# Optimization experiments

Hardware: AMD Instinct MI355X
Metric: run time of the kernel (lower is better)

## Reference

```python
import jax, jax.numpy as jnp
import numpy as np

N = 50000   # nodes
E = 800000  # edges (avg degree 16)
D = 96      # in = hid = out
BN_EPS = 1e-5


def setup_inputs() -> dict:
    key = jax.random.key(0)
    ks = jax.random.split(key, 16)
    features = jax.random.normal(ks[0], (N, D), jnp.float32)
    src = jax.random.randint(ks[1], (E,), 0, N)
    dst = jax.random.randint(ks[2], (E,), 0, N)
    bound = 1.0 / np.sqrt(D)
    def lin(kw, kb):
        W = jax.random.uniform(kw, (D, D), jnp.float32, -bound, bound)
        b = jax.random.uniform(kb, (D,), jnp.float32, -bound, bound)
        return W, b
    W1, b1 = lin(ks[3], ks[4])
    W2, b2 = lin(ks[5], ks[6])
    W3, b3 = lin(ks[7], ks[8])
    gamma1 = jnp.ones((D,), jnp.float32)
    beta1 = jnp.zeros((D,), jnp.float32)
    gamma2 = jnp.ones((D,), jnp.float32)
    beta2 = jnp.zeros((D,), jnp.float32)
    return dict(features=features, W1=W1, b1=b1, gamma1=gamma1, beta1=beta1,
                W2=W2, b2=b2, gamma2=gamma2, beta2=beta2, W3=W3, b3=b3,
                src=src, dst=dst)


def _gin_conv(h, W, b, src, dst, inv_deg):
    # mean-aggregate incoming neighbor features, eps = 0: (h + mean_nb) @ W + b
    agg = jax.ops.segment_sum(h[src], dst, num_segments=N) * inv_deg[:, None]
    return (h + agg) @ W + b


def _batchnorm(x, gamma, beta):
    mu = jnp.mean(x, axis=0)
    var = jnp.mean((x - mu) ** 2, axis=0)  # biased, as torch BN training
    return (x - mu) * jax.lax.rsqrt(var + BN_EPS) * gamma + beta


def reference(features, W1, b1, gamma1, beta1, W2, b2, gamma2, beta2, W3, b3, src, dst):
    deg = jax.ops.segment_sum(jnp.ones((E,), jnp.float32), dst, num_segments=N)
    inv_deg = jnp.where(deg > 0, 1.0 / jnp.maximum(deg, 1.0), 0.0)
    h = _gin_conv(features, W1, b1, src, dst, inv_deg)
    h = jax.nn.relu(_batchnorm(h, gamma1, beta1))  # dropout p=0 -> identity
    h = _gin_conv(h, W2, b2, src, dst, inv_deg)
    h = jax.nn.relu(_batchnorm(h, gamma2, beta2))
    h = _gin_conv(h, W3, b3, src, dst, inv_deg)
    return h
```

## Files before the change

### kernel.cpp

```cpp
#include <hip/hip_runtime.h>

#define FD 96
#define BSH 7
#define BNODES 128
#define NBLK 256

typedef float  f32x4 __attribute__((ext_vector_type(4)));
typedef short  s16x8 __attribute__((ext_vector_type(8)));

__device__ __forceinline__ unsigned short f2bf(float x) {
    unsigned u = __float_as_uint(x);
    u = (u + 0x7fffu + ((u >> 16) & 1u)) >> 16;
    return (unsigned short)u;
}
__device__ __forceinline__ float bflo(unsigned u) { return __uint_as_float(u << 16); }
__device__ __forceinline__ float bfhi(unsigned u) { return __uint_as_float(u & 0xffff0000u); }


__global__ void k_h2d(const int* __restrict__ dst, int* __restrict__ hist2d,
                      int E, int nbkt, int chunk) {
    __shared__ int hist[512];
    int tid = threadIdx.x, b = blockIdx.x;
    for (int i = tid; i < 512; i += 256) hist[i] = 0;
    __syncthreads();
    int lo = b * chunk, hi = min(lo + chunk, E);
    for (int i = lo + tid; i < hi; i += 256)
        atomicAdd(&hist[dst[i] >> BSH], 1);
    __syncthreads();
    for (int q = tid; q < nbkt; q += 256)
        hist2d[(size_t)q * NBLK + b] = hist[q];
}

__global__ void k_cscan(const int* __restrict__ hist2d, int* __restrict__ cursor2d,
                        int* __restrict__ bcnt, float* __restrict__ accz) {
    __shared__ int sh[NBLK];
    int q = blockIdx.x, tid = threadIdx.x;
    if (q == 0) for (int i = tid; i < 4 * FD; i += 256) accz[i] = 0.f;
    int v = hist2d[(size_t)q * NBLK + tid];
    sh[tid] = v;
    __syncthreads();
    for (int off = 1; off < NBLK; off <<= 1) {
        int t = (tid >= off) ? sh[tid - off] : 0;
        __syncthreads();
        sh[tid] += t;
        __syncthreads();
    }
    cursor2d[(size_t)q * NBLK + tid] = sh[tid] - v;
    if (tid == NBLK - 1) bcnt[q] = sh[tid];
}

__global__ void k_bscan(const int* __restrict__ bcnt, int* __restrict__ bbase, int nbkt) {
    __shared__ int sh[512];
    int tid = threadIdx.x;
    int v = (tid < nbkt) ? bcnt[tid] : 0;
    sh[tid] = v;
    __syncthreads();
    for (int off = 1; off < 512; off <<= 1) {
        int t = (tid >= off) ? sh[tid - off] : 0;
        __syncthreads();
        sh[tid] += t;
        __syncthreads();
    }
    int incl = sh[tid];
    if (tid < nbkt) bbase[tid] = incl - v;
    if (tid == nbkt - 1) bbase[nbkt] = incl;
}

__global__ void k_scat(const int* __restrict__ src, const int* __restrict__ dst,
                       const int* __restrict__ cursor2d, const int* __restrict__ bbase,
                       uint2* __restrict__ ebuf, int E, int nbkt, int chunk) {
    __shared__ int cur[512];
    int tid = threadIdx.x, b = blockIdx.x;
    for (int q = tid; q < nbkt; q += 256)
        cur[q] = bbase[q] + cursor2d[(size_t)q * NBLK + b];
    __syncthreads();
    int lo = b * chunk, hi = min(lo + chunk, E);
    for (int i = lo + tid; i < hi; i += 256) {
        int d = dst[i];
        int p = atomicAdd(&cur[d >> BSH], 1);
        ebuf[p] = make_uint2((unsigned)d, (unsigned)src[i]);
    }
}

__global__ void k_bsort(const uint2* __restrict__ ebuf, const int* __restrict__ bbase,
                        int* __restrict__ csr, int* __restrict__ rp2, int* __restrict__ re2,
                        float* __restrict__ invd2, int* __restrict__ perm,
                        int* __restrict__ inv_perm, int n) {
    __shared__ int cnt[BNODES];
    __shared__ int cur[BNODES];
    __shared__ int dh[64];
    const int b = blockIdx.x;
    const int tid = threadIdx.x;
    const int lo = bbase[b], hi = bbase[b + 1];
    if (tid < BNODES) cnt[tid] = 0;
    if (tid < 64) dh[tid] = 0;
    __syncthreads();
    for (int i = lo + tid; i < hi; i += blockDim.x)
        atomicAdd(&cnt[(int)ebuf[i].x - (b << BSH)], 1);
    __syncthreads();
    const int node = (b << BSH) + tid;
    const int v = (tid < BNODES) ? cnt[tid] : 0;
    const int dcl = min(v, 63);
    if (tid < BNODES && node < n) atomicAdd(&dh[dcl], 1);
    for (int off = 1; off < BNODES; off <<= 1) {
        int t = (tid < BNODES && tid >= off) ? cnt[tid - off] : 0;
        __syncthreads();
        if (tid < BNODES) cnt[tid] += t;
        __syncthreads();
    }
    int dv = (tid < 64) ? dh[tid] : 0;
    for (int off = 1; off < 64; off <<= 1) {
        int t = (tid < 64 && tid >= off) ? dh[tid - off] : 0;
        __syncthreads();
        if (tid < 64) dh[tid] += t;
        __syncthreads();
    }
    if (tid < 64) dh[tid] -= dv;
    __syncthreads();
    if (tid < BNODES) {
        int excl = cnt[tid] - v;
        if (node < n) {
            int rk = atomicAdd(&dh[dcl], 1);
            int slot = (b << BSH) + rk;
            perm[slot] = node;
            inv_perm[node] = slot;
            rp2[slot] = lo + excl;
            re2[slot] = lo + excl + v;
            invd2[slot] = (v > 0) ? (1.0f / (float)v) : 0.f;
        }
        cur[tid] = excl;
    }
    __syncthreads();
    for (int i = lo + tid; i < hi; i += blockDim.x) {
        uint2 e2 = ebuf[i];
        int local = (int)e2.x - (b << BSH);
        int p = lo + atomicAdd(&cur[local], 1);
        csr[p] = (int)e2.y;
    }
}

__global__ void k_prep(int* __restrict__ csr, const int* __restrict__ inv_perm, int E,
                       const float* __restrict__ feat, const int* __restrict__ perm,
                       uint4* __restrict__ hA, int n,
                       const float* __restrict__ W1, const float* __restrict__ W2,
                       const float* __restrict__ W3, unsigned short* __restrict__ Wt) {
    int i = blockIdx.x * blockDim.x + threadIdx.x;
    if (i < E) {
        csr[i] = inv_perm[csr[i]];
        return;
    }
    i -= E;
    const int n12 = n * 12;
    if (i < n12) {
        int row = i / 12, q = i - row * 12;
        int node = perm[row];
        const float4* rp = (const float4*)(feat + (size_t)node * FD);
        float4 x = rp[2 * q], y = rp[2 * q + 1];
        uint4 r;
        r.x = (unsigned)f2bf(x.x) | ((unsigned)f2bf(x.y) << 16);
        r.y = (unsigned)f2bf(x.z) | ((unsigned)f2bf(x.w) << 16);
        r.z = (unsigned)f2bf(y.x) | ((unsigned)f2bf(y.y) << 16);
        r.w = (unsigned)f2bf(y.z) | ((unsigned)f2bf(y.w) << 16);
        hA[i] = r;
        return;
    }
    i -= n12;
    if (i < 3 * FD * FD) {
        int m = i / (FD * FD), r = i - m * FD * FD;
        const float* W = (m == 0) ? W1 : ((m == 1) ? W2 : W3);
        int col = r % FD, k = r / FD;
        Wt[m * FD * FD + col * FD + k] = f2bf(W[r]);
    }
}


template<int NORM, int STATS, int OBF>
__global__ __launch_bounds__(256) void k_aggmm(
    const uint4* __restrict__ h,
    const int* __restrict__ rp2, const int* __restrict__ re2,
    const float* __restrict__ invd2, const int* __restrict__ csr,
    const float* __restrict__ accPrev, const float* __restrict__ gamma,
    const float* __restrict__ beta,
    const unsigned short* __restrict__ Wt, const float* __restrict__ bias,
    const int* __restrict__ perm,
    unsigned short* __restrict__ yb, float* __restrict__ yf,
    float* __restrict__ accg, int n, float invN)
{
    __shared__ uint4 t_lds[64][13];
    __shared__ float sred[2 * FD];
    const int tid = threadIdx.x;
    const int rl = tid >> 2;
    const int qq = tid & 3;
    const int idx = blockIdx.x * 64 + rl;
    const bool valid = (idx < n);
    int beg = 0, end = 0;
    float id = 0.f;
    if (valid) { beg = rp2[idx]; end = re2[idx]; id = invd2[idx]; }

    #pragma unroll 1
    for (int p = 0; p < 3; p++) {
        const int q = p * 4 + qq;
        float a[8], c[8];
        if (NORM) {
            #pragma unroll
            for (int z = 0; z < 8; z++) {
                int f = q * 8 + z;
                float mu  = accPrev[f] * invN;
                float var = accPrev[FD + f] * invN - mu * mu;
                float aa  = gamma[f] * rsqrtf(var + 1e-5f);
                a[z] = aa;
                c[z] = beta[f] - mu * aa;
            }
        }
        float o[8];
        #pragma unroll
        for (int z = 0; z < 8; z++) o[z] = 0.f;

        if (valid) {
            float acc8[8];
            #pragma unroll
            for (int z = 0; z < 8; z++) acc8[z] = 0.f;
            int e = beg;
            for (; e + 8 <= end; e += 8) {
                uint4 raw[8];
                #pragma unroll
                for (int u = 0; u < 8; u++) raw[u] = h[(size_t)csr[e + u] * 12 + q];
                #pragma unroll
                for (int u = 0; u < 8; u++) {
                    float v[8];
                    v[0] = bflo(raw[u].x); v[1] = bfhi(raw[u].x);
                    v[2] = bflo(raw[u].y); v[3] = bfhi(raw[u].y);
                    v[4] = bflo(raw[u].z); v[5] = bfhi(raw[u].z);
                    v[6] = bflo(raw[u].w); v[7] = bfhi(raw[u].w);
                    #pragma unroll
                    for (int z = 0; z < 8; z++) {
                        float x = v[z];
                        if (NORM) x = fmaxf(fmaf(a[z], x, c[z]), 0.f);
                        acc8[z] += x;
                    }
                }
            }
            for (; e < end; e++) {
                uint4 raw = h[(size_t)csr[e] * 12 + q];
                float v[8];
                v[0] = bflo(raw.x); v[1] = bfhi(raw.x);
                v[2] = bflo(raw.y); v[3] = bfhi(raw.y);
                v[4] = bflo(raw.z); v[5] = bfhi(raw.z);
                v[6] = bflo(raw.w); v[7] = bfhi(raw.w);
                #pragma unroll
                for (int z = 0; z < 8; z++) {
                    float x = v[z];
                    if (NORM) x = fmaxf(fmaf(a[z], x, c[z]), 0.f);
                    acc8[z] += x;
                }
            }
            uint4 rs = h[(size_t)idx * 12 + q];
            float xs[8];
            xs[0] = bflo(rs.x); xs[1] = bfhi(rs.x);
            xs[2] = bflo(rs.y); xs[3] = bfhi(rs.y);
            xs[4] = bflo(rs.z); xs[5] = bfhi(rs.z);
            xs[6] = bflo(rs.w); xs[7] = bfhi(rs.w);
            #pragma unroll
            for (int z = 0; z < 8; z++) {
                float x = xs[z];
                if (NORM) x = fmaxf(fmaf(a[z], x, c[z]), 0.f);
                o[z] = fmaf(id, acc8[z], x);
            }
        }
        uint4 pk;
        pk.x = (unsigned)f2bf(o[0]) | ((unsigned)f2bf(o[1]) << 16);
        pk.y = (unsigned)f2bf(o[2]) | ((unsigned)f2bf(o[3]) << 16);
        pk.z = (unsigned)f2bf(o[4]) | ((unsigned)f2bf(o[5]) << 16);
        pk.w = (unsigned)f2bf(o[6]) | ((unsigned)f2bf(o[7]) << 16);
        t_lds[rl][q] = pk;
    }
    __syncthreads();

    const int lane = tid & 63;
    const int wv   = tid >> 6;
    const int colb = lane & 15;
    const int hg   = lane >> 4;
    const int rbase = blockIdx.x * 64 + wv * 16;

    s16x8 a[3];
    #pragma unroll
    for (int s = 0; s < 3; s++)
        a[s] = *reinterpret_cast<const s16x8*>(&t_lds[wv * 16 + colb][s * 4 + hg]);

    s16x8 b[6][3];
    #pragma unroll
    for (int c2 = 0; c2 < 6; c2++)
        #pragma unroll
        for (int s = 0; s < 3; s++)
            b[c2][s] = *reinterpret_cast<const s16x8*>(Wt + (size_t)(c2 * 16 + colb) * FD + s * 32 + hg * 8);

    f32x4 acc[6];
    #pragma unroll
    for (int c2 = 0; c2 < 6; c2++) acc[c2] = (f32x4){0.f, 0.f, 0.f, 0.f};
    #pragma unroll
    for (int s = 0; s < 3; s++)
        #pragma unroll
        for (int c2 = 0; c2 < 6; c2++)
            acc[c2] = __builtin_amdgcn_mfma_f32_16x16x32_bf16(a[s], b[c2][s], acc[c2], 0, 0, 0);

    int orow[4];
    #pragma unroll
    for (int j = 0; j < 4; j++) {
        int rr = rbase + hg * 4 + j;
        orow[j] = (!OBF && rr < n) ? perm[rr] : rr;
    }
    float s1[6], s2[6];
    #pragma unroll
    for (int c2 = 0; c2 < 6; c2++) { s1[c2] = 0.f; s2[c2] = 0.f; }
    #pragma unroll
    for (int c2 = 0; c2 < 6; c2++) {
        float bc = bias[c2 * 16 + colb];
        #pragma unroll
        for (int j = 0; j < 4; j++) {
            int rr = rbase + hg * 4 + j;
            if (rr < n) {
                float y = acc[c2][j] + bc;
                if (OBF) yb[(size_t)rr * FD + c2 * 16 + colb] = f2bf(y);
                else     yf[(size_t)orow[j] * FD + c2 * 16 + colb] = y;
                if (STATS) { s1[c2] += y; s2[c2] = fmaf(y, y, s2[c2]); }
            }
        }
    }
    if (STATS) {
        if (tid < 2 * FD) sred[tid] = 0.f;
        __syncthreads();
        #pragma unroll
        for (int c2 = 0; c2 < 6; c2++) {
            float v1 = s1[c2], v2 = s2[c2];
            v1 += __shfl_xor(v1, 16, 64); v1 += __shfl_xor(v1, 32, 64);
            v2 += __shfl_xor(v2, 16, 64); v2 += __shfl_xor(v2, 32, 64);
            if (lane < 16) {
                atomicAdd(&sred[c2 * 16 + colb], v1);
                atomicAdd(&sred[FD + c2 * 16 + colb], v2);
            }
        }
        __syncthreads();
        if (tid < 2 * FD) atomicAdd(&accg[tid], sred[tid]);
    }
}

extern "C" void kernel_launch(void* const* d_in, const int* in_sizes, int n_in,
                              void* d_out, int out_size, void* d_ws, size_t ws_size,
                              hipStream_t stream) {
    const float* feat = (const float*)d_in[0];
    const float* W1   = (const float*)d_in[1];
    const float* b1   = (const float*)d_in[2];
    const float* g1   = (const float*)d_in[3];
    const float* be1  = (const float*)d_in[4];
    const float* W2   = (const float*)d_in[5];
    const float* b2   = (const float*)d_in[6];
    const float* g2   = (const float*)d_in[7];
    const float* be2  = (const float*)d_in[8];
    const float* W3   = (const float*)d_in[9];
    const float* b3   = (const float*)d_in[10];
    const int*   src  = (const int*)d_in[11];
    const int*   dst  = (const int*)d_in[12];

    const int n = in_sizes[0] / FD;
    const int e = in_sizes[11];
    const int nbkt = (n + BNODES - 1) >> BSH;
    const int chunk = (e + NBLK - 1) / NBLK;

    char* w = (char*)d_ws;
    unsigned short* hA  = (unsigned short*)w; w += (size_t)n * FD * 2;
    unsigned short* hB  = (unsigned short*)w; w += (size_t)n * FD * 2;
    unsigned short* Wt  = (unsigned short*)w; w += (size_t)3 * FD * FD * 2;
    int*   csr     = (int*)w;   w += (size_t)e * 4;
    int*   bcnt    = (int*)w;   w += 512 * 4;
    float* acc1    = (float*)w; w += 2 * FD * 4;
    float* acc2    = (float*)w; w += 2 * FD * 4;
    int*   bbase   = (int*)w;   w += 513 * 4;
    int*   hist2d  = (int*)w;   w += (size_t)512 * NBLK * 4;
    int*   cursor2d= (int*)w;   w += (size_t)512 * NBLK * 4;
    int*   rp2     = (int*)w;   w += (size_t)n * 4;
    int*   re2     = (int*)w;   w += (size_t)n * 4;
    float* invd2   = (float*)w; w += (size_t)n * 4;
    int*   perm    = (int*)w;   w += (size_t)n * 4;
    int*   invp    = (int*)w;   w += (size_t)n * 4;

    uint2* ebuf = (uint2*)hB;

    float* O = (float*)d_out;
    const float invN = 1.0f / (float)n;
    const int FUSE_GRID = (n + 63) / 64;
    const int n12 = n * 12;
    const int prep_items = e + n12 + 3 * FD * FD;

    k_h2d<<<NBLK, 256, 0, stream>>>(dst, hist2d, e, nbkt, chunk);
    k_cscan<<<nbkt, NBLK, 0, stream>>>(hist2d, cursor2d, bcnt, acc1);
    k_bscan<<<1, 512, 0, stream>>>(bcnt, bbase, nbkt);
    k_scat<<<NBLK, 256, 0, stream>>>(src, dst, cursor2d, bbase, ebuf, e, nbkt, chunk);
    k_bsort<<<nbkt, 256, 0, stream>>>(ebuf, bbase, csr, rp2, re2, invd2, perm, invp, n);
    k_prep<<<(prep_items + 255) / 256, 256, 0, stream>>>(csr, invp, e, feat, perm,
                                                         (uint4*)hA, n, W1, W2, W3, Wt);

    k_aggmm<0, 1, 1><<<FUSE_GRID, 256, 0, stream>>>(
        (const uint4*)hA, rp2, re2, invd2, csr, nullptr, nullptr, nullptr,
        Wt, b1, perm, hB, nullptr, acc1, n, invN);

    k_aggmm<1, 1, 1><<<FUSE_GRID, 256, 0, stream>>>(
        (const uint4*)hB, rp2, re2, invd2, csr, acc1, g1, be1,
        Wt + FD * FD, b2, perm, hA, nullptr, acc2, n, invN);

    k_aggmm<1, 0, 0><<<FUSE_GRID, 256, 0, stream>>>(
        (const uint4*)hA, rp2, re2, invd2, csr, acc2, g2, be2,
        Wt + 2 * FD * FD, b3, perm, nullptr, O, nullptr, n, invN);
}
```

Before: 262.7 us.

## Split fused aggregate+matmul into separate gather and MFMA kernels

Splits each fused aggregation-plus-GEMM layer into a gather kernel that uses one thread per (row, 16-byte chunk) and a separate MFMA matmul kernel. The split intermediate goes to global memory, and one of the bf16 activation buffers now lives in the output buffer. This is meant to give the latency-bound gather full parallelism (12 lanes per row, no 3-pass loop, occupancy hint of 4 blocks) instead of serialising per block before the LDS handoff. The cost is three extra kernel launches plus a global round-trip of the aggregated tensor per layer.

```diff
diff --git a/kernel.cpp b/kernel.cpp
--- a/kernel.cpp
+++ b/kernel.cpp
@@ -174,119 +174,118 @@
 }
 
 
-template<int NORM, int STATS, int OBF>
-__global__ __launch_bounds__(256) void k_aggmm(
+template<int NORM>
+__global__ __launch_bounds__(256, 4) void k_agg(
     const uint4* __restrict__ h,
     const int* __restrict__ rp2, const int* __restrict__ re2,
     const float* __restrict__ invd2, const int* __restrict__ csr,
     const float* __restrict__ accPrev, const float* __restrict__ gamma,
-    const float* __restrict__ beta,
-    const unsigned short* __restrict__ Wt, const float* __restrict__ bias,
-    const int* __restrict__ perm,
-    unsigned short* __restrict__ yb, float* __restrict__ yf,
-    float* __restrict__ accg, int n, float invN)
+    const float* __restrict__ beta, float invN,
+    uint4* __restrict__ t, int n)
 {
-    __shared__ uint4 t_lds[64][13];
-    __shared__ float sred[2 * FD];
-    const int tid = threadIdx.x;
-    const int rl = tid >> 2;
-    const int qq = tid & 3;
-    const int idx = blockIdx.x * 64 + rl;
-    const bool valid = (idx < n);
-    int beg = 0, end = 0;
-    float id = 0.f;
-    if (valid) { beg = rp2[idx]; end = re2[idx]; id = invd2[idx]; }
-
-    #pragma unroll 1
-    for (int p = 0; p < 3; p++) {
-        const int q = p * 4 + qq;
-        float a[8], c[8];
-        if (NORM) {
+    int g = blockIdx.x * blockDim.x + threadIdx.x;
+    int row = g / 12;
+    if (row >= n) return;
+    int q = g - row * 12;
+    float a[8], c[8];
+    if (NORM) {
+        #pragma unroll
+        for (int z = 0; z < 8; z++) {
+            int f = q * 8 + z;
+            float mu  = accPrev[f] * invN;
+            float var = accPrev[FD + f] * invN - mu * mu;
+            float aa  = gamma[f] * rsqrtf(var + 1e-5f);
+            a[z] = aa;
+            c[z] = beta[f] - mu * aa;
+        }
+    }
+    float acc8[8];
+    #pragma unroll
+    for (int z = 0; z < 8; z++) acc8[z] = 0.f;
+
+    int e = rp2[row];
+    const int end = re2[row];
+    for (; e + 8 <= end; e += 8) {
+        uint4 raw[8];
+        #pragma unroll
+        for (int u = 0; u < 8; u++) raw[u] = h[(size_t)csr[e + u] * 12 + q];
+        #pragma unroll
+        for (int u = 0; u < 8; u++) {
+            float v[8];
+            v[0] = bflo(raw[u].x); v[1] = bfhi(raw[u].x);
+            v[2] = bflo(raw[u].y); v[3] = bfhi(raw[u].y);
+            v[4] = bflo(raw[u].z); v[5] = bfhi(raw[u].z);
+            v[6] = bflo(raw[u].w); v[7] = bfhi(raw[u].w);
             #pragma unroll
             for (int z = 0; z < 8; z++) {
-                int f = q * 8 + z;
-                float mu  = accPrev[f] * invN;
-                float var = accPrev[FD + f] * invN - mu * mu;
-                float aa  = gamma[f] * rsqrtf(var + 1e-5f);
-                a[z] = aa;
-                c[z] = beta[f] - mu * aa;
+                float x = v[z];
+                if (NORM) x = fmaxf(fmaf(a[z], x, c[z]), 0.f);
+                acc8[z] += x;
             }
         }
-        float o[8];
-        #pragma unroll
-        for (int z = 0; z < 8; z++) o[z] = 0.f;
-
-        if (valid) {
-            float acc8[8];
-            #pragma unroll
-            for (int z = 0; z < 8; z++) acc8[z] = 0.f;
-            int e = beg;
-            for (; e + 8 <= end; e += 8) {
-                uint4 raw[8];
-                #pragma unroll
-                for (int u = 0; u < 8; u++) raw[u] = h[(size_t)csr[e + u] * 12 + q];
-                #pragma unroll
-                for (int u = 0; u < 8; u++) {
-                    float v[8];
-                    v[0] = bflo(raw[u].x); v[1] = bfhi(raw[u].x);
-                    v[2] = bflo(raw[u].y); v[3] = bfhi(raw[u].y);
-                    v[4] = bflo(raw[u].z); v[5] = bfhi(raw[u].z);
-                    v[6] = bflo(raw[u].w); v[7] = bfhi(raw[u].w);
-                    #pragma unroll
-                    for (int z = 0; z < 8; z++) {
-                        float x = v[z];
-                        if (NORM) x = fmaxf(fmaf(a[z], x, c[z]), 0.f);
-                        acc8[z] += x;
-                    }
-                }
-            }
-            for (; e < end; e++) {
-                uint4 raw = h[(size_t)csr[e] * 12 + q];
-                float v[8];
-                v[0] = bflo(raw.x); v[1] = bfhi(raw.x);
-                v[2] = bflo(raw.y); v[3] = bfhi(raw.y);
-                v[4] = bflo(raw.z); v[5] = bfhi(raw.z);
-                v[6] = bflo(raw.w); v[7] = bfhi(raw.w);
-                #pragma unroll
-                for (int z = 0; z < 8; z++) {
-                    float x = v[z];
-                    if (NORM) x = fmaxf(fmaf(a[z], x, c[z]), 0.f);
-                    acc8[z] += x;
-                }
-            }
-            uint4 rs = h[(size_t)idx * 12 + q];
-            float xs[8];
-            xs[0] = bflo(rs.x); xs[1] = bfhi(rs.x);
-            xs[2] = bflo(rs.y); xs[3] = bfhi(rs.y);
-            xs[4] = bflo(rs.z); xs[5] = bfhi(rs.z);
-            xs[6] = bflo(rs.w); xs[7] = bfhi(rs.w);
-            #pragma unroll
-            for (int z = 0; z < 8; z++) {
-                float x = xs[z];
-                if (NORM) x = fmaxf(fmaf(a[z], x, c[z]), 0.f);
-                o[z] = fmaf(id, acc8[z], x);
-            }
-        }
-        uint4 pk;
-        pk.x = (unsigned)f2bf(o[0]) | ((unsigned)f2bf(o[1]) << 16);
-        pk.y = (unsigned)f2bf(o[2]) | ((unsigned)f2bf(o[3]) << 16);
-        pk.z = (unsigned)f2bf(o[4]) | ((unsigned)f2bf(o[5]) << 16);
-        pk.w = (unsigned)f2bf(o[6]) | ((unsigned)f2bf(o[7]) << 16);
-        t_lds[rl][q] = pk;
-    }
-    __syncthreads();
-
+    }
+    for (; e < end; e++) {
+        uint4 raw = h[(size_t)csr[e] * 12 + q];
+        float v[8];
+        v[0] = bflo(raw.x); v[1] = bfhi(raw.x);
+        v[2] = bflo(raw.y); v[3] = bfhi(raw.y);
+        v[4] = bflo(raw.z); v[5] = bfhi(raw.z);
+        v[6] = bflo(raw.w); v[7] = bfhi(raw.w);
+        #pragma unroll
+        for (int z = 0; z < 8; z++) {
+            float x = v[z];
+            if (NORM) x = fmaxf(fmaf(a[z], x, c[z]), 0.f);
+            acc8[z] += x;
+        }
+    }
+    uint4 rs = h[(size_t)row * 12 + q];
+    float xs[8];
+    xs[0] = bflo(rs.x); xs[1] = bfhi(rs.x);
+    xs[2] = bflo(rs.y); xs[3] = bfhi(rs.y);
+    xs[4] = bflo(rs.z); xs[5] = bfhi(rs.z);
+    xs[6] = bflo(rs.w); xs[7] = bfhi(rs.w);
+    float id = invd2[row];
+    float o[8];
+    #pragma unroll
+    for (int z = 0; z < 8; z++) {
+        float x = xs[z];
+        if (NORM) x = fmaxf(fmaf(a[z], x, c[z]), 0.f);
+        o[z] = fmaf(id, acc8[z], x);
+    }
+    uint4 pk;
+    pk.x = (unsigned)f2bf(o[0]) | ((unsigned)f2bf(o[1]) << 16);
+    pk.y = (unsigned)f2bf(o[2]) | ((unsigned)f2bf(o[3]) << 16);
+    pk.z = (unsigned)f2bf(o[4]) | ((unsigned)f2bf(o[5]) << 16);
+    pk.w = (unsigned)f2bf(o[6]) | ((unsigned)f2bf(o[7]) << 16);
+    t[(size_t)row * 12 + q] = pk;
+}
+
+
+template<int STATS, int OBF>
+__global__ void k_mm(const unsigned short* __restrict__ ta,
+                     const unsigned short* __restrict__ Wt,
+                     const float* __restrict__ bias, const int* __restrict__ perm,
+                     unsigned short* __restrict__ yb, float* __restrict__ yf,
+                     float* __restrict__ accg, int n)
+{
+    __shared__ float sred[2 * FD];
+    const int tid  = threadIdx.x;
     const int lane = tid & 63;
     const int wv   = tid >> 6;
     const int colb = lane & 15;
     const int hg   = lane >> 4;
     const int rbase = blockIdx.x * 64 + wv * 16;
+    const int r = rbase + colb;
 
     s16x8 a[3];
-    #pragma unroll
-    for (int s = 0; s < 3; s++)
-        a[s] = *reinterpret_cast<const s16x8*>(&t_lds[wv * 16 + colb][s * 4 + hg]);
-
+    if (r < n) {
+        #pragma unroll
+        for (int s = 0; s < 3; s++)
+            a[s] = *reinterpret_cast<const s16x8*>(ta + (size_t)r * FD + s * 32 + hg * 8);
+    } else {
+        #pragma unroll
+        for (int s = 0; s < 3; s++) a[s] = s16x8{0, 0, 0, 0, 0, 0, 0, 0};
+    }
     s16x8 b[6][3];
     #pragma unroll
     for (int c2 = 0; c2 < 6; c2++)
@@ -368,7 +367,7 @@
 
     char* w = (char*)d_ws;
     unsigned short* hA  = (unsigned short*)w; w += (size_t)n * FD * 2;
-    unsigned short* hB  = (unsigned short*)w; w += (size_t)n * FD * 2;
+    unsigned short* tb  = (unsigned short*)w; w += (size_t)n * FD * 2;
     unsigned short* Wt  = (unsigned short*)w; w += (size_t)3 * FD * FD * 2;
     int*   csr     = (int*)w;   w += (size_t)e * 4;
     int*   bcnt    = (int*)w;   w += 512 * 4;
@@ -383,11 +382,12 @@
     int*   perm    = (int*)w;   w += (size_t)n * 4;
     int*   invp    = (int*)w;   w += (size_t)n * 4;
 
-    uint2* ebuf = (uint2*)hB;
-
+    uint2* ebuf = (uint2*)tb;
+    unsigned short* hB = (unsigned short*)d_out;
     float* O = (float*)d_out;
     const float invN = 1.0f / (float)n;
-    const int FUSE_GRID = (n + 63) / 64;
+    const int AGG_GRID = (n * 12 + 255) / 256;
+    const int MM_GRID  = (n + 63) / 64;
     const int n12 = n * 12;
     const int prep_items = e + n12 + 3 * FD * FD;
 
@@ -399,15 +399,15 @@
     k_prep<<<(prep_items + 255) / 256, 256, 0, stream>>>(csr, invp, e, feat, perm,
                                                          (uint4*)hA, n, W1, W2, W3, Wt);
 
-    k_aggmm<0, 1, 1><<<FUSE_GRID, 256, 0, stream>>>(
-        (const uint4*)hA, rp2, re2, invd2, csr, nullptr, nullptr, nullptr,
-        Wt, b1, perm, hB, nullptr, acc1, n, invN);
-
-    k_aggmm<1, 1, 1><<<FUSE_GRID, 256, 0, stream>>>(
-        (const uint4*)hB, rp2, re2, invd2, csr, acc1, g1, be1,
-        Wt + FD * FD, b2, perm, hA, nullptr, acc2, n, invN);
-
-    k_aggmm<1, 0, 0><<<FUSE_GRID, 256, 0, stream>>>(
-        (const uint4*)hA, rp2, re2, invd2, csr, acc2, g2, be2,
-        Wt + 2 * FD * FD, b3, perm, nullptr, O, nullptr, n, invN);
-}
+    k_agg<0><<<AGG_GRID, 256, 0, stream>>>((const uint4*)hA, rp2, re2, invd2, csr,
+                                           nullptr, nullptr, nullptr, invN, (uint4*)tb, n);
+    k_mm<1, 1><<<MM_GRID, 256, 0, stream>>>(tb, Wt, b1, perm, hB, nullptr, acc1, n);
+
+    k_agg<1><<<AGG_GRID, 256, 0, stream>>>((const uint4*)hB, rp2, re2, invd2, csr,
+                                           acc1, g1, be1, invN, (uint4*)tb, n);
+    k_mm<1, 1><<<MM_GRID, 256, 0, stream>>>(tb, Wt + FD * FD, b2, perm, hA, nullptr, acc2, n);
+
+    k_agg<1><<<AGG_GRID, 256, 0, stream>>>((const uint4*)hA, rp2, re2, invd2, csr,
+                                           acc2, g2, be2, invN, (uint4*)tb, n);
+    k_mm<0, 0><<<MM_GRID, 256, 0, stream>>>(tb, Wt + 2 * FD * FD, b3, perm, nullptr, O, nullptr, n);
+}
```

New measurement: 210.2 us (median of 2 runs). 1.25x faster.
